# Kernel tuning notes

Measured on AMD Instinct MI355X. Metric: run time of the kernel, lower is better.

## Reference

```python
import jax, jax.numpy as jnp
from jax import lax
import numpy as np

L, QD, B = 16, 2048, 4096


def setup_inputs() -> dict:
    key = jax.random.key(0)
    k1, k2, k3, k4 = jax.random.split(key, 4)
    input_state = jax.random.normal(k1, (B, QD), dtype=jnp.float32)
    # rotation_angles ~ U(-0.1, 0.1) per _initialize_parameters
    rotation_angles = jax.random.uniform(k2, (L, QD, 3), dtype=jnp.float32, minval=-0.1, maxval=0.1)
    # xavier_uniform for [qd, qd] weights: bound = sqrt(6 / (qd + qd))
    bound = float(np.sqrt(6.0 / (QD + QD)))
    entanglement_weights = jax.random.uniform(k3, (L, QD, QD), dtype=jnp.float32, minval=-bound, maxval=bound)
    # orthogonal init for measurement basis via QR
    m = jax.random.normal(k4, (QD, QD), dtype=jnp.float32)
    q, r = jnp.linalg.qr(m)
    measurement_basis = (q * jnp.sign(jnp.diagonal(r))).astype(jnp.float32)
    return {
        "input_state": input_state,
        "rotation_angles": rotation_angles,
        "entanglement_weights": entanglement_weights,
        "measurement_basis": measurement_basis,
    }


def reference(input_state, rotation_angles, entanglement_weights, measurement_basis):
    # Each rotation gate reduces to an elementwise scale by cos(angle/2):
    #   x-gate: real(rot[0,0]) = cos(a/2); y-gate: cos(a/2); z-gate: real(exp(-i a/2)) = cos(a/2).
    # Fuse all three gates per layer into one per-dim scale: [L, QD]
    scales = jnp.prod(jnp.cos(rotation_angles * 0.5), axis=-1)

    def layer_step(state, layer_params):
        scale, w = layer_params  # scale: [QD], w: [QD, QD]
        return jnp.matmul(state * scale, w), None

    state, _ = lax.scan(layer_step, input_state, (scales, entanglement_weights))
    return jnp.matmul(state, measurement_basis)
```

## Files before the change

### kernel.cpp

```cpp
#include <hip/hip_runtime.h>
#include <stdint.h>

#define L_LAYERS 16
#define QD 2048
#define BATCH 4096

typedef __attribute__((ext_vector_type(8))) __bf16 bf16x8;
typedef __attribute__((ext_vector_type(4))) float f32x4;
typedef __attribute__((address_space(3))) uint32_t lds32_t;
typedef const __attribute__((address_space(1))) uint32_t glob32_t;

__device__ __forceinline__ void async_load16(const void* g, void* l) {
    __builtin_amdgcn_global_load_lds((glob32_t*)(uintptr_t)g, (lds32_t*)(uintptr_t)l,
                                     16, 0, 0);
}

__device__ __forceinline__ unsigned short f2bf(float f) {
    uint32_t u = __float_as_uint(f);
    u += 0x7FFFu + ((u >> 16) & 1u);
    return (unsigned short)(u >> 16);
}

__global__ void scales_kernel(const float* __restrict__ ang, float* __restrict__ sc, int n) {
    int i = blockIdx.x * 256 + threadIdx.x;
    if (i < n) {
        float a0 = ang[3 * i + 0], a1 = ang[3 * i + 1], a2 = ang[3 * i + 2];
        sc[i] = __cosf(a0 * 0.5f) * __cosf(a1 * 0.5f) * __cosf(a2 * 0.5f);
    }
}

__global__ void convert_in_kernel(const float* __restrict__ in,
                                  unsigned short* __restrict__ out, int n4) {
    int i = blockIdx.x * 256 + threadIdx.x;
    if (i < n4) {
        float4 v = ((const float4*)in)[i];
        ushort4 o;
        o.x = f2bf(v.x); o.y = f2bf(v.y); o.z = f2bf(v.z); o.w = f2bf(v.w);
        ((ushort4*)out)[i] = o;
    }
}

__global__ void convert_a_all(const float* __restrict__ W, const float* __restrict__ sc,
                              unsigned short* __restrict__ out) {
    const int z = blockIdx.z;
    const float* src = W + (size_t)(2 * z) * QD * QD;
    const float* srow = sc + (2 * z) * QD;
    unsigned short* dst = out + (size_t)z * QD * QD;
    int i = blockIdx.x * 256 + threadIdx.x;
    float s = srow[i >> 9];
    float4 v = ((const float4*)src)[i];
    ushort4 o;
    o.x = f2bf(v.x * s); o.y = f2bf(v.y * s); o.z = f2bf(v.z * s); o.w = f2bf(v.w * s);
    ((ushort4*)dst)[i] = o;
}

__device__ __forceinline__ void conv_tile_body(const float* __restrict__ src,
                                               const float* __restrict__ srow,
                                               unsigned short* __restrict__ dst) {
    __shared__ __align__(16) unsigned short tile[64][72];
    const int t = threadIdx.x;
    const int k0 = blockIdx.y * 64, n0 = blockIdx.x * 64;
    const int r = t >> 4;
    const int c = (t & 15) * 4;
#pragma unroll
    for (int rr = 0; rr < 64; rr += 16) {
        int k = k0 + r + rr;
        float s = srow ? srow[k] : 1.0f;
        float4 v = *(const float4*)(src + (size_t)k * QD + n0 + c);
        tile[c + 0][r + rr] = f2bf(v.x * s);
        tile[c + 1][r + rr] = f2bf(v.y * s);
        tile[c + 2][r + rr] = f2bf(v.z * s);
        tile[c + 3][r + rr] = f2bf(v.w * s);
    }
    __syncthreads();
    const int wr = t >> 3;
    const int wc = (t & 7) * 8;
#pragma unroll
    for (int rr = 0; rr < 64; rr += 32) {
        *(float4*)(dst + (size_t)(n0 + wr + rr) * QD + k0 + wc) =
            *(const float4*)(&tile[wr + rr][wc]);
    }
}

__global__ void convert_b_all(const float* __restrict__ W, const float* __restrict__ Mb,
                              const float* __restrict__ sc, unsigned short* __restrict__ out) {
    const int z = blockIdx.z;
    const float* src = (z < 8) ? (W + (size_t)(2 * z + 1) * QD * QD) : Mb;
    const float* srow = (z < 8) ? (sc + (2 * z + 1) * QD) : nullptr;
    unsigned short* dst = out + (size_t)z * QD * QD;
    conv_tile_body(src, srow, dst);
}

struct GemmBatch {
    const unsigned short* a[8];
    const unsigned short* b[8];
    void* c[8];
};

template <int OUT_BF16, int TM>
__global__ __launch_bounds__(256, TM == 128 ? 2 : 4)
void gemm_kernel(GemmBatch args) {
    constexpr int NI = TM / 32;
    __shared__ __align__(16) unsigned short ldsA[TM * 64];
    __shared__ __align__(16) unsigned short ldsB[128 * 64];
    const unsigned short* __restrict__ A  = args.a[blockIdx.z];
    const unsigned short* __restrict__ Bt = args.b[blockIdx.z];
    void* __restrict__ Cout = args.c[blockIdx.z];

    const int t = threadIdx.x;
    const int n0 = blockIdx.x * 128;
    const int m0 = blockIdx.y * TM;
    const int lane = t & 63;
    const int wave = t >> 6;
    const int wm = (wave & 1) * (TM / 2);
    const int wn = (wave >> 1) * 64;
    const int fr = lane & 15;
    const int quad = lane >> 4;

    f32x4 acc[NI][4] = {};

    const int sr = t >> 2;
    const int scol = (t & 3) * 8;
    const unsigned short* ga = A + (size_t)(m0 + sr) * QD + scol;
    const unsigned short* gb = Bt + (size_t)(n0 + sr) * QD + scol;
    unsigned short* la = ldsA + t * 8;
    unsigned short* lb = ldsB + t * 8;

    for (int k0 = 0; k0 < QD; k0 += 64) {
        __syncthreads();
        if constexpr (TM == 128) {
            async_load16(ga, la);
            async_load16(ga + 64 * QD, la + 2048);
            async_load16(ga + 32, la + 4096);
            async_load16(ga + 32 + 64 * QD, la + 6144);
        } else {
            async_load16(ga, la);
            async_load16(ga + 32, la + 2048);
        }
        async_load16(gb, lb);
        async_load16(gb + 64 * QD, lb + 2048);
        async_load16(gb + 32, lb + 4096);
        async_load16(gb + 32 + 64 * QD, lb + 6144);
        ga += 64;
        gb += 64;
        __syncthreads();

#pragma unroll
        for (int kk = 0; kk < 2; kk++) {
            const unsigned short* pa = ldsA + kk * (TM * 32);
            const unsigned short* pb = ldsB + kk * 4096;
            bf16x8 af[NI], bfr[4];
#pragma unroll
            for (int i = 0; i < NI; i++)
                af[i] = *(const bf16x8*)(pa + (wm + i * 16 + fr) * 32 + quad * 8);
#pragma unroll
            for (int j = 0; j < 4; j++)
                bfr[j] = *(const bf16x8*)(pb + (wn + j * 16 + fr) * 32 + quad * 8);
#pragma unroll
            for (int i = 0; i < NI; i++)
#pragma unroll
                for (int j = 0; j < 4; j++)
                    acc[i][j] = __builtin_amdgcn_mfma_f32_16x16x32_bf16(af[i], bfr[j],
                                                                        acc[i][j], 0, 0, 0);
        }
    }

#pragma unroll
    for (int i = 0; i < NI; i++) {
        const int gr = m0 + wm + i * 16 + quad * 4;
#pragma unroll
        for (int j = 0; j < 4; j++) {
            const int gc = n0 + wn + j * 16 + fr;
#pragma unroll
            for (int r = 0; r < 4; r++) {
                float v = acc[i][j][r];
                if (OUT_BF16)
                    ((unsigned short*)Cout)[(size_t)(gr + r) * QD + gc] = f2bf(v);
                else
                    ((float*)Cout)[(size_t)(gr + r) * QD + gc] = v;
            }
        }
    }
}

extern "C" void kernel_launch(void* const* d_in, const int* in_sizes, int n_in,
                              void* d_out, int out_size, void* d_ws, size_t ws_size,
                              hipStream_t stream) {
    const float* input_state = (const float*)d_in[0];
    const float* angles      = (const float*)d_in[1];
    const float* W           = (const float*)d_in[2];
    const float* Mb          = (const float*)d_in[3];

    const size_t mat = (size_t)QD * QD;
    char* ws = (char*)d_ws;
    float* scales = (float*)ws;
    size_t off = 131072;
    unsigned short* xb = (unsigned short*)(ws + off); off += (size_t)BATCH * QD * 2;
    unsigned short* WA = (unsigned short*)(ws + off); off += 8 * mat * 2;
    unsigned short* WB = (unsigned short*)(ws + off); off += 9 * mat * 2;
    unsigned short* T1 = (unsigned short*)(ws + off); off += 8 * mat * 2;
    unsigned short* T2 = (unsigned short*)(ws + off); off += 4 * mat * 2;
    unsigned short* T3 = (unsigned short*)(ws + off); off += 2 * mat * 2;
    unsigned short* T4 = (unsigned short*)(ws + off); off += mat * 2;
    unsigned short* T5 = (unsigned short*)(ws + off); off += mat * 2;

    scales_kernel<<<(L_LAYERS * QD + 255) / 256, 256, 0, stream>>>(angles, scales,
                                                                   L_LAYERS * QD);
    convert_in_kernel<<<(BATCH * QD / 4) / 256, 256, 0, stream>>>(input_state, xb,
                                                                  BATCH * QD / 4);
    convert_a_all<<<dim3(mat / 4 / 256, 1, 8), 256, 0, stream>>>(W, scales, WA);
    convert_b_all<<<dim3(QD / 64, QD / 64, 9), 256, 0, stream>>>(W, Mb, scales, WB);

    GemmBatch b1{};
    for (int i = 0; i < 8; i++) {
        const unsigned short* wa = WA + (size_t)i * mat;
        const unsigned short* wb = WB + (size_t)i * mat;
        if ((i & 1) == 0) { b1.a[i] = wa; b1.b[i] = wb; }
        else              { b1.a[i] = wb; b1.b[i] = wa; }
        b1.c[i] = T1 + (size_t)i * mat;
    }
    gemm_kernel<1, 128><<<dim3(QD / 128, QD / 128, 8), 256, 0, stream>>>(b1);

    GemmBatch b2{};
    for (int i = 0; i < 4; i++) {
        b2.a[i] = T1 + (size_t)(2 * i + (i & 1)) * mat;
        b2.b[i] = T1 + (size_t)(2 * i + 1 - (i & 1)) * mat;
        b2.c[i] = T2 + (size_t)i * mat;
    }
    gemm_kernel<1, 128><<<dim3(QD / 128, QD / 128, 4), 256, 0, stream>>>(b2);

    GemmBatch b3{};
    for (int i = 0; i < 2; i++) {
        b3.a[i] = T2 + (size_t)(2 * i + (i & 1)) * mat;
        b3.b[i] = T2 + (size_t)(2 * i + 1 - (i & 1)) * mat;
        b3.c[i] = T3 + (size_t)i * mat;
    }
    gemm_kernel<1, 128><<<dim3(QD / 128, QD / 128, 2), 256, 0, stream>>>(b3);

    GemmBatch b4{};
    b4.a[0] = T3; b4.b[0] = T3 + mat; b4.c[0] = T4;
    gemm_kernel<1, 64><<<dim3(QD / 128, QD / 64, 1), 256, 0, stream>>>(b4);

    GemmBatch b5{};
    b5.a[0] = WB + 8 * mat; b5.b[0] = T4; b5.c[0] = T5;
    gemm_kernel<1, 64><<<dim3(QD / 128, QD / 64, 1), 256, 0, stream>>>(b5);

    GemmBatch ba{};
    ba.a[0] = xb; ba.b[0] = T5; ba.c[0] = d_out;
    gemm_kernel<0, 128><<<dim3(QD / 128, BATCH / 128, 1), 256, 0, stream>>>(ba);
}
```

Baseline: 785.1 us.

## Add 256x256-tile 8-wave GEMM kernel with interleaved prefetch for product-tree stages

Adds a new bf16 MFMA GEMM kernel that computes a 256x256 output tile per 512-thread block. It double-buffers 64-wide K slices in LDS, issuing async global-to-LDS loads for the next slice between the four MFMA sub-phases, and raises wave priority during the MFMA bursts. The first two batched stages of the weight-matrix product tree now use it instead of the 128x128 kernel, to get more data reuse per LDS byte and to overlap loads with compute. The cost is 128KB of LDS per block and fewer blocks per stage, which can reduce occupancy, especially in the 4-matrix stage (256 blocks).

```diff
diff --git a/kernel.cpp b/kernel.cpp
--- a/kernel.cpp
+++ b/kernel.cpp
@@ -183,6 +183,159 @@
     }
 }
 
+__device__ __forceinline__ void stage_half(const unsigned short* __restrict__ G,
+                                           int row0, int k0,
+                                           unsigned char* dst, int t) {
+    const int r = t >> 3;
+    const int c = ((t & 7) * 8) ^ (((t >> 5) & 1) * 16);
+    const unsigned short* g = G + (size_t)(row0 + r) * QD + k0 + c;
+    async_load16(g, dst + t * 16);
+    async_load16(g + 64 * QD, dst + 8192 + t * 16);
+}
+
+template <int OUT_BF16>
+__global__ __launch_bounds__(512, 2)
+void gemm256_kernel(GemmBatch args) {
+    __shared__ __align__(16) unsigned char lds[131072];
+    const unsigned short* __restrict__ A  = args.a[blockIdx.z];
+    const unsigned short* __restrict__ Bt = args.b[blockIdx.z];
+    void* __restrict__ Cout = args.c[blockIdx.z];
+
+    const int t = threadIdx.x;
+    const int lane = t & 63;
+    const int wid = t >> 6;
+    const int wm = (wid >> 2) * 128;
+    const int wn = (wid & 3) * 64;
+    const int fr = lane & 15;
+    const int quad = lane >> 4;
+    const int m0 = blockIdx.y * 256;
+    const int n0 = blockIdx.x * 256;
+
+    unsigned char* ldsA8 = lds;
+    unsigned char* ldsB8 = lds + 65536;
+    const int swz = ((fr >> 2) & 1) << 5;
+    const unsigned char* sA = ldsA8 + (wm >> 7) * 16384 + fr * 128 + ((quad * 16) ^ swz);
+    const unsigned char* sB = ldsB8 + ((wn >> 7) & 1) * 16384 + (wn & 64) * 128
+                              + fr * 128 + ((quad * 16) ^ swz);
+
+    f32x4 acc[8][4] = {};
+    bf16x8 af[4][2], bfA[2][2], bfB[2][2];
+
+    constexpr int NT = QD / 64;
+
+    stage_half(A,  m0,       0,  ldsA8,         t);
+    stage_half(A,  m0 + 128, 0,  ldsA8 + 16384, t);
+    stage_half(Bt, n0,       0,  ldsB8,         t);
+    stage_half(Bt, n0 + 128, 0,  ldsB8 + 16384, t);
+    stage_half(A,  m0,       64, ldsA8 + 32768, t);
+    stage_half(Bt, n0,       64, ldsB8 + 32768, t);
+    asm volatile("s_waitcnt vmcnt(4)" ::: "memory");
+    __builtin_amdgcn_s_barrier();
+
+    for (int kt = 0; kt < NT; ++kt) {
+        const int buf  = (kt & 1) << 15;
+        const int nbuf = (~kt & 1) << 15;
+        const int k1 = ((kt + 1) & (NT - 1)) << 6;
+        const int k2 = ((kt + 2) & (NT - 1)) << 6;
+
+#pragma unroll
+        for (int mf = 0; mf < 4; mf++)
+#pragma unroll
+            for (int kk = 0; kk < 2; kk++)
+                af[mf][kk] = *(const bf16x8*)(sA + buf + mf * 2048 + kk * 64);
+#pragma unroll
+        for (int nf = 0; nf < 2; nf++)
+#pragma unroll
+            for (int kk = 0; kk < 2; kk++)
+                bfA[nf][kk] = *(const bf16x8*)(sB + buf + nf * 2048 + kk * 64);
+        stage_half(A, m0 + 128, k1, ldsA8 + nbuf + 16384, t);
+        __builtin_amdgcn_s_barrier();
+        __builtin_amdgcn_s_setprio(1);
+#pragma unroll
+        for (int mf = 0; mf < 4; mf++)
+#pragma unroll
+            for (int nf = 0; nf < 2; nf++)
+#pragma unroll
+                for (int kk = 0; kk < 2; kk++)
+                    acc[mf][nf] = __builtin_amdgcn_mfma_f32_16x16x32_bf16(
+                        af[mf][kk], bfA[nf][kk], acc[mf][nf], 0, 0, 0);
+        __builtin_amdgcn_s_setprio(0);
+        __builtin_amdgcn_s_barrier();
+
+#pragma unroll
+        for (int nf = 0; nf < 2; nf++)
+#pragma unroll
+            for (int kk = 0; kk < 2; kk++)
+                bfB[nf][kk] = *(const bf16x8*)(sB + buf + (nf + 2) * 2048 + kk * 64);
+        stage_half(Bt, n0 + 128, k1, ldsB8 + nbuf + 16384, t);
+        __builtin_amdgcn_s_barrier();
+        __builtin_amdgcn_s_setprio(1);
+#pragma unroll
+        for (int mf = 0; mf < 4; mf++)
+#pragma unroll
+            for (int nf = 0; nf < 2; nf++)
+#pragma unroll
+                for (int kk = 0; kk < 2; kk++)
+                    acc[mf][nf + 2] = __builtin_amdgcn_mfma_f32_16x16x32_bf16(
+                        af[mf][kk], bfB[nf][kk], acc[mf][nf + 2], 0, 0, 0);
+        __builtin_amdgcn_s_setprio(0);
+        __builtin_amdgcn_s_barrier();
+
+#pragma unroll
+        for (int mf = 0; mf < 4; mf++)
+#pragma unroll
+            for (int kk = 0; kk < 2; kk++)
+                af[mf][kk] = *(const bf16x8*)(sA + buf + (mf + 4) * 2048 + kk * 64);
+        stage_half(Bt, n0, k2, ldsB8 + buf, t);
+        __builtin_amdgcn_s_barrier();
+        __builtin_amdgcn_s_setprio(1);
+#pragma unroll
+        for (int mf = 0; mf < 4; mf++)
+#pragma unroll
+            for (int nf = 0; nf < 2; nf++)
+#pragma unroll
+                for (int kk = 0; kk < 2; kk++)
+                    acc[mf + 4][nf + 2] = __builtin_amdgcn_mfma_f32_16x16x32_bf16(
+                        af[mf][kk], bfB[nf][kk], acc[mf + 4][nf + 2], 0, 0, 0);
+        __builtin_amdgcn_s_setprio(0);
+        __builtin_amdgcn_s_barrier();
+
+        stage_half(A, m0, k2, ldsA8 + buf, t);
+        __builtin_amdgcn_s_barrier();
+        __builtin_amdgcn_s_setprio(1);
+#pragma unroll
+        for (int mf = 0; mf < 4; mf++)
+#pragma unroll
+            for (int nf = 0; nf < 2; nf++)
+#pragma unroll
+                for (int kk = 0; kk < 2; kk++)
+                    acc[mf + 4][nf] = __builtin_amdgcn_mfma_f32_16x16x32_bf16(
+                        af[mf][kk], bfA[nf][kk], acc[mf + 4][nf], 0, 0, 0);
+        __builtin_amdgcn_s_setprio(0);
+        asm volatile("s_waitcnt vmcnt(4)" ::: "memory");
+        __builtin_amdgcn_s_barrier();
+    }
+
+    asm volatile("s_waitcnt vmcnt(0)" ::: "memory");
+
+#pragma unroll
+    for (int mf = 0; mf < 8; mf++) {
+        const int gr = m0 + wm + mf * 16 + quad * 4;
+#pragma unroll
+        for (int nf = 0; nf < 4; nf++) {
+            const int gc = n0 + wn + nf * 16 + fr;
+#pragma unroll
+            for (int r = 0; r < 4; r++) {
+                float v = acc[mf][nf][r];
+                if (OUT_BF16)
+                    ((unsigned short*)Cout)[(size_t)(gr + r) * QD + gc] = f2bf(v);
+                else
+                    ((float*)Cout)[(size_t)(gr + r) * QD + gc] = v;
+            }
+        }
+    }
+}
+
 extern "C" void kernel_launch(void* const* d_in, const int* in_sizes, int n_in,
                               void* d_out, int out_size, void* d_ws, size_t ws_size,
                               hipStream_t stream) {
@@ -219,7 +372,7 @@
         else              { b1.a[i] = wb; b1.b[i] = wa; }
         b1.c[i] = T1 + (size_t)i * mat;
     }
-    gemm_kernel<1, 128><<<dim3(QD / 128, QD / 128, 8), 256, 0, stream>>>(b1);
+    gemm256_kernel<1><<<dim3(QD / 256, QD / 256, 8), 512, 0, stream>>>(b1);
 
     GemmBatch b2{};
     for (int i = 0; i < 4; i++) {
@@ -227,7 +380,7 @@
         b2.b[i] = T1 + (size_t)(2 * i + 1 - (i & 1)) * mat;
         b2.c[i] = T2 + (size_t)i * mat;
     }
-    gemm_kernel<1, 128><<<dim3(QD / 128, QD / 128, 4), 256, 0, stream>>>(b2);
+    gemm256_kernel<1><<<dim3(QD / 256, QD / 256, 4), 512, 0, stream>>>(b2);
 
     GemmBatch b3{};
     for (int i = 0; i < 2; i++) {
```

New measurement: 769.5 us. 2.0% less time.
